# Kernel tuning notes

Measured on AMD Instinct MI355X. Metric: run time of the kernel, lower is better.

The kernel has to match this reference:

```python
import jax, jax.numpy as jnp
import numpy as np

B, T, J, C = 8, 243, 17, 512
H = 8
HD = C // H  # 64
SCALE = HD ** -0.5


def setup_inputs() -> dict:
    key = jax.random.key(0)
    ks = jax.random.split(key, 6)
    x = jax.random.normal(ks[0], (B, T, J, C), dtype=jnp.float32)
    # external attention map, broadcast-compatible with [B,H,J,T,T]; make it row-normalized like a softmax
    am = jax.random.uniform(ks[1], (B, H, J, T, T), dtype=jnp.float32)
    att_map = am / jnp.sum(am, axis=-1, keepdims=True)
    weight = jax.random.uniform(ks[2], (1,), dtype=jnp.float32)
    w_qkv = jax.random.normal(ks[3], (3 * C, C), dtype=jnp.float32) * 0.02
    w_proj = jax.random.normal(ks[4], (C, C), dtype=jnp.float32) * 0.02
    b_proj = jax.random.normal(ks[5], (C,), dtype=jnp.float32) * 0.02
    return {"x": x, "att_map": att_map, "weight": weight,
            "w_qkv": w_qkv, "w_proj": w_proj, "b_proj": b_proj}


def reference(x, att_map, weight, w_qkv, w_proj, b_proj):
    b, t, j, c = x.shape
    h, hd = H, c // H
    # qkv projection (no bias): [B,T,J,3C] -> [3,B,H,T,J,hd]
    qkv = jnp.einsum('btjc,dc->btjd', x, w_qkv).reshape(b, t, j, 3, h, hd)
    qkv = jnp.transpose(qkv, (3, 0, 4, 1, 2, 5))
    q, k, v = qkv[0], qkv[1], qkv[2]
    # transpose T <-> J: attention runs over the temporal axis per joint
    qt = jnp.swapaxes(q, 2, 3)  # [B,H,J,T,hd]
    kt = jnp.swapaxes(k, 2, 3)
    vt = jnp.swapaxes(v, 2, 3)
    attn = jnp.einsum('bhjtc,bhjsc->bhjts', qt, kt) * SCALE  # [B,H,J,T,T]
    attn = jax.nn.softmax(attn, axis=-1)
    # blend with external attention map (dropout p=0.0 -> identity)
    attn = weight * attn + (1.0 - weight) * att_map
    out = jnp.einsum('bhjts,bhjsc->bhjtc', attn, vt)  # [B,H,J,T,hd]
    out = jnp.transpose(out, (0, 3, 2, 1, 4)).reshape(b, t, j, c)  # [B,T,J,C]
    out = out @ w_proj.T + b_proj
    return out
```

## Files before the change

kernel.cpp:

```cpp
#include <hip/hip_runtime.h>
#include <hip/hip_bf16.h>

#define B_ 8
#define T_ 243
#define J_ 17
#define C_ 512
#define H_ 8
#define HD_ 64
#define M_ (B_*T_*J_)
#define SCALE_ 0.125f
#define QKV_ELEMS (B_*H_*J_*T_*HD_)

typedef __attribute__((ext_vector_type(4))) float f32x4;
typedef __attribute__((ext_vector_type(8))) short bf16x8;

__device__ __forceinline__ ushort f2bf(float f) {
  union { float f; unsigned u; } v; v.f = f;
  unsigned r = v.u + 0x7FFFu + ((v.u >> 16) & 1u);
  return (ushort)(r >> 16);
}
__device__ __forceinline__ float bf2f(ushort u) {
  union { unsigned u; float f; } v; v.u = (unsigned)u << 16; return v.f;
}
__device__ __forceinline__ int vchunk(int g, int row) {
  return g ^ (row & 7) ^ ((row >> 3) & 7);
}

__global__ __launch_bounds__(256) void cvt_kernel(const float* __restrict__ in,
                                                  ushort* __restrict__ out, int n8) {
  int i = blockIdx.x * 256 + threadIdx.x;
  if (i >= n8) return;
  const float4* p = (const float4*)in + (size_t)i * 2;
  float4 v0 = p[0], v1 = p[1];
  bf16x8 o;
  o[0] = (short)f2bf(v0.x); o[1] = (short)f2bf(v0.y);
  o[2] = (short)f2bf(v0.z); o[3] = (short)f2bf(v0.w);
  o[4] = (short)f2bf(v1.x); o[5] = (short)f2bf(v1.y);
  o[6] = (short)f2bf(v1.z); o[7] = (short)f2bf(v1.w);
  *(bf16x8*)(out + (size_t)i * 8) = o;
}

template<int EPI>
__global__ __launch_bounds__(256) void gemm_bt(
    const ushort* __restrict__ A, const ushort* __restrict__ Bm,
    ushort* __restrict__ qkvout, float* __restrict__ fout,
    const float* __restrict__ bias)
{
  __shared__ ushort As[128 * 64];
  __shared__ ushort Bs[128 * 64];
  const int tid = threadIdx.x;
  const int lane = tid & 63;
  const int lo = lane & 15, hi = lane >> 4;
  const int wave = tid >> 6;
  const int wr = wave >> 1, wc = wave & 1;
  const int mt = blockIdx.x, nt = blockIdx.y;

  f32x4 acc[4][4] = {};

  for (int ks = 0; ks < 8; ++ks) {
    const int k0 = ks * 64;
    bf16x8 ra[4], rb[4];
    #pragma unroll
    for (int i = 0; i < 4; ++i) {
      int c = tid + i * 256;
      int row = c >> 3, col8 = c & 7;
      int arow = mt * 128 + row; if (arow > M_ - 1) arow = M_ - 1;
      ra[i] = *(const bf16x8*)(A + (size_t)arow * 512 + k0 + col8 * 8);
      int brow = nt * 128 + row;
      rb[i] = *(const bf16x8*)(Bm + (size_t)brow * 512 + k0 + col8 * 8);
    }
    __syncthreads();
    #pragma unroll
    for (int i = 0; i < 4; ++i) {
      int c = tid + i * 256;
      int row = c >> 3, col8 = c & 7;
      int sc = col8 ^ (row & 7);
      *(bf16x8*)(As + row * 64 + sc * 8) = ra[i];
      *(bf16x8*)(Bs + row * 64 + sc * 8) = rb[i];
    }
    __syncthreads();
    #pragma unroll
    for (int kk = 0; kk < 2; ++kk) {
      bf16x8 af[4], bf[4];
      #pragma unroll
      for (int mf = 0; mf < 4; ++mf) {
        int row = wr * 64 + mf * 16 + lo;
        int sc = (kk * 4 + hi) ^ (row & 7);
        af[mf] = *(const bf16x8*)(As + row * 64 + sc * 8);
      }
      #pragma unroll
      for (int nf = 0; nf < 4; ++nf) {
        int row = wc * 64 + nf * 16 + lo;
        int sc = (kk * 4 + hi) ^ (row & 7);
        bf[nf] = *(const bf16x8*)(Bs + row * 64 + sc * 8);
      }
      #pragma unroll
      for (int mf = 0; mf < 4; ++mf)
        #pragma unroll
        for (int nf = 0; nf < 4; ++nf)
          acc[mf][nf] = __builtin_amdgcn_mfma_f32_16x16x32_bf16(af[mf], bf[nf], acc[mf][nf], 0, 0, 0);
    }
  }

  if (EPI == 0) {
    const int which = nt >> 2;
    const int h = (nt * 2 + wc) & 7;
    const float scale = (which == 0) ? SCALE_ : 1.0f;
    ushort* basep = qkvout + (size_t)which * QKV_ELEMS;
    #pragma unroll
    for (int mf = 0; mf < 4; ++mf) {
      #pragma unroll
      for (int i = 0; i < 4; ++i) {
        int r = mt * 128 + wr * 64 + mf * 16 + hi * 4 + i;
        if (r >= M_) continue;
        int b = r / (T_ * J_);
        int rem = r - b * (T_ * J_);
        int t = rem / J_;
        int j = rem - t * J_;
        size_t rowoff = (((size_t)(b * H_ + h) * J_ + j) * T_ + t) * HD_;
        #pragma unroll
        for (int nf = 0; nf < 4; ++nf) {
          int hd = nf * 16 + lo;
          basep[rowoff + hd] = f2bf(acc[mf][nf][i] * scale);
        }
      }
    }
  } else {
    #pragma unroll
    for (int mf = 0; mf < 4; ++mf) {
      #pragma unroll
      for (int i = 0; i < 4; ++i) {
        int r = mt * 128 + wr * 64 + mf * 16 + hi * 4 + i;
        if (r >= M_) continue;
        #pragma unroll
        for (int nf = 0; nf < 4; ++nf) {
          int n = nt * 128 + wc * 64 + nf * 16 + lo;
          fout[(size_t)r * C_ + n] = acc[mf][nf][i] + bias[n];
        }
      }
    }
  }
}

__global__ __launch_bounds__(256, 3) void attn_kernel(
    const ushort* __restrict__ q, const ushort* __restrict__ k,
    const ushort* __restrict__ v, const float* __restrict__ am,
    const float* __restrict__ wptr, ushort* __restrict__ outO)
{
  __shared__ ushort Vt[64 * 256];
  __shared__ ushort Ps[64 * 128];
  __shared__ float red0[2][64];
  __shared__ float red1[2][64];

  const int tid = threadIdx.x;
  const int lane = tid & 63;
  const int lo = lane & 15, hi = lane >> 4;
  const int wave = tid >> 6;
  const int wr = wave >> 1, wc = wave & 1;
  const int bid = blockIdx.x;
  const int workid = (bid & 7) * 544 + (bid >> 3);
  const int bhj = workid >> 2, rt = workid & 3;
  const int bh = bhj / J_, j = bhj - bh * J_;
  const int b = bh >> 3, h = bh & 7;
  const float w = wptr[0];
  const float wb = 1.0f - w;
  const size_t kvbase = (size_t)bhj * (T_ * HD_);
  const int r0 = rt * 64;

  #pragma unroll
  for (int it = 0; it < 8; ++it) {
    int c = tid + it * 256;
    int s = c >> 3, hd0 = (c & 7) * 8;
    bf16x8 val = {};
    if (s < T_) val = *(const bf16x8*)(v + kvbase + (size_t)s * HD_ + hd0);
    #pragma unroll
    for (int e = 0; e < 8; ++e) {
      int row = hd0 + e;
      int chunk = vchunk(s >> 3, row);
      Vt[row * 256 + chunk * 8 + (s & 7)] = (ushort)val[e];
    }
  }
  __syncthreads();

  bf16x8 aq[2][2];
  #pragma unroll
  for (int mf = 0; mf < 2; ++mf) {
    int t = r0 + wr * 32 + mf * 16 + lo; if (t > T_ - 1) t = T_ - 1;
    #pragma unroll
    for (int kk = 0; kk < 2; ++kk)
      aq[mf][kk] = *(const bf16x8*)(q + kvbase + (size_t)t * HD_ + kk * 32 + hi * 8);
  }

  f32x4 acc[2][8] = {};
  #pragma unroll
  for (int nf = 0; nf < 8; ++nf) {
    int s = wc * 128 + nf * 16 + lo; if (s > T_ - 1) s = T_ - 1;
    #pragma unroll
    for (int kk = 0; kk < 2; ++kk) {
      bf16x8 bk = *(const bf16x8*)(k + kvbase + (size_t)s * HD_ + kk * 32 + hi * 8);
      #pragma unroll
      for (int mf = 0; mf < 2; ++mf)
        acc[mf][nf] = __builtin_amdgcn_mfma_f32_16x16x32_bf16(aq[mf][kk], bk, acc[mf][nf], 0, 0, 0);
    }
  }

  float rmax[2][4];
  #pragma unroll
  for (int mf = 0; mf < 2; ++mf)
    #pragma unroll
    for (int i = 0; i < 4; ++i) {
      float m = -1e30f;
      #pragma unroll
      for (int nf = 0; nf < 8; ++nf) {
        int s = wc * 128 + nf * 16 + lo;
        if (s < T_) m = fmaxf(m, acc[mf][nf][i]);
      }
      rmax[mf][i] = m;
    }
  #pragma unroll
  for (int d = 1; d < 16; d <<= 1)
    #pragma unroll
    for (int mf = 0; mf < 2; ++mf)
      #pragma unroll
      for (int i = 0; i < 4; ++i)
        rmax[mf][i] = fmaxf(rmax[mf][i], __shfl_xor(rmax[mf][i], d, 64));
  if (lo == 0) {
    #pragma unroll
    for (int mf = 0; mf < 2; ++mf)
      #pragma unroll
      for (int i = 0; i < 4; ++i)
        red0[wc][wr * 32 + mf * 16 + hi * 4 + i] = rmax[mf][i];
  }
  __syncthreads();

  float rsum[2][4];
  #pragma unroll
  for (int mf = 0; mf < 2; ++mf)
    #pragma unroll
    for (int i = 0; i < 4; ++i) {
      float Mx = fmaxf(rmax[mf][i], red0[wc ^ 1][wr * 32 + mf * 16 + hi * 4 + i]);
      float ssum = 0.f;
      #pragma unroll
      for (int nf = 0; nf < 8; ++nf) {
        int s = wc * 128 + nf * 16 + lo;
        float e = 0.f;
        if (s < T_) e = __expf(acc[mf][nf][i] - Mx);
        acc[mf][nf][i] = e;
        ssum += e;
      }
      rsum[mf][i] = ssum;
    }
  #pragma unroll
  for (int d = 1; d < 16; d <<= 1)
    #pragma unroll
    for (int mf = 0; mf < 2; ++mf)
      #pragma unroll
      for (int i = 0; i < 4; ++i)
        rsum[mf][i] += __shfl_xor(rsum[mf][i], d, 64);
  if (lo == 0) {
    #pragma unroll
    for (int mf = 0; mf < 2; ++mf)
      #pragma unroll
      for (int i = 0; i < 4; ++i)
        red1[wc][wr * 32 + mf * 16 + hi * 4 + i] = rsum[mf][i];
  }
  __syncthreads();

  float pinv[2][4];
  #pragma unroll
  for (int mf = 0; mf < 2; ++mf)
    #pragma unroll
    for (int i = 0; i < 4; ++i) {
      float L = rsum[mf][i] + red1[wc ^ 1][wr * 32 + mf * 16 + hi * 4 + i];
      pinv[mf][i] = w / L;
    }

  f32x4 oacc[2][2] = {};
  #pragma unroll
  for (int h2 = 0; h2 < 2; ++h2) {
    __syncthreads();
    if (wc == h2) {
      #pragma unroll
      for (int mf = 0; mf < 2; ++mf)
        #pragma unroll
        for (int i = 0; i < 4; ++i) {
          int row_local = wr * 32 + mf * 16 + hi * 4 + i;
          float pw = pinv[mf][i];
          #pragma unroll
          for (int nf = 0; nf < 8; ++nf) {
            int s = h2 * 128 + nf * 16 + lo;
            float p = (s < T_) ? acc[mf][nf][i] * pw : 0.f;
            int s_local = nf * 16 + lo;
            int chunk = (s_local >> 3) ^ (row_local & 7);
            Ps[row_local * 128 + chunk * 8 + (s_local & 7)] = f2bf(p);
          }
        }
    }
    __syncthreads();
    #pragma unroll
    for (int kk = 0; kk < 4; ++kk) {
      bf16x8 ap[2], bv[2];
      #pragma unroll
      for (int mf = 0; mf < 2; ++mf) {
        int row = wr * 32 + mf * 16 + lo;
        int chunk = (kk * 4 + hi) ^ (row & 7);
        ap[mf] = *(const bf16x8*)(Ps + row * 128 + chunk * 8);
      }
      #pragma unroll
      for (int nf = 0; nf < 2; ++nf) {
        int row = wc * 32 + nf * 16 + lo;
        int chunk = vchunk((h2 * 4 + kk) * 4 + hi, row);
        bv[nf] = *(const bf16x8*)(Vt + row * 256 + chunk * 8);
      }
      #pragma unroll
      for (int mf = 0; mf < 2; ++mf)
        #pragma unroll
        for (int nf = 0; nf < 2; ++nf)
          oacc[mf][nf] = __builtin_amdgcn_mfma_f32_16x16x32_bf16(ap[mf], bv[nf], oacc[mf][nf], 0, 0, 0);
    }
  }

  const float* amrow[2];
  #pragma unroll
  for (int mf = 0; mf < 2; ++mf) {
    int t = r0 + wr * 32 + mf * 16 + lo; if (t > T_ - 1) t = T_ - 1;
    amrow[mf] = am + (size_t)bhj * (T_ * T_) + (size_t)t * T_;
  }
  f32x4 amacc[2][2] = {};
  #pragma unroll
  for (int kk = 0; kk < 8; ++kk) {
    const int s8 = kk * 32 + hi * 8;
    bf16x8 aa[2];
    #pragma unroll
    for (int mf = 0; mf < 2; ++mf) {
      bf16x8 r;
      if (s8 + 7 <= T_ - 1) {
        #pragma unroll
        for (int e = 0; e < 8; ++e) r[e] = (short)f2bf(amrow[mf][s8 + e]);
      } else {
        #pragma unroll
        for (int e = 0; e < 8; ++e) {
          int s = s8 + e;
          r[e] = (s <= T_ - 1) ? (short)f2bf(amrow[mf][s]) : (short)0;
        }
      }
      aa[mf] = r;
    }
    bf16x8 bv[2];
    #pragma unroll
    for (int nf = 0; nf < 2; ++nf) {
      int row = wc * 32 + nf * 16 + lo;
      int chunk = vchunk(kk * 4 + hi, row);
      bv[nf] = *(const bf16x8*)(Vt + row * 256 + chunk * 8);
    }
    #pragma unroll
    for (int mf = 0; mf < 2; ++mf)
      #pragma unroll
      for (int nf = 0; nf < 2; ++nf)
        amacc[mf][nf] = __builtin_amdgcn_mfma_f32_16x16x32_bf16(aa[mf], bv[nf], amacc[mf][nf], 0, 0, 0);
  }

  #pragma unroll
  for (int mf = 0; mf < 2; ++mf)
    #pragma unroll
    for (int i = 0; i < 4; ++i) {
      int t = r0 + wr * 32 + mf * 16 + hi * 4 + i;
      if (t >= T_) continue;
      size_t orow = ((size_t)(b * T_ + t) * J_ + j) * C_ + h * HD_;
      #pragma unroll
      for (int nf = 0; nf < 2; ++nf) {
        int hd = wc * 32 + nf * 16 + lo;
        outO[orow + hd] = f2bf(oacc[mf][nf][i] + wb * amacc[mf][nf][i]);
      }
    }
}

extern "C" void kernel_launch(void* const* d_in, const int* in_sizes, int n_in,
                              void* d_out, int out_size, void* d_ws, size_t ws_size,
                              hipStream_t stream) {
  const float* x      = (const float*)d_in[0];
  const float* am     = (const float*)d_in[1];
  const float* weight = (const float*)d_in[2];
  const float* w_qkv  = (const float*)d_in[3];
  const float* w_proj = (const float*)d_in[4];
  const float* b_proj = (const float*)d_in[5];
  float* outp = (float*)d_out;

  char* ws = (char*)d_ws;
  ushort* wqkv_bf  = (ushort*)(ws);
  ushort* wproj_bf = (ushort*)(ws + 1572864);
  ushort* xbf      = (ushort*)(ws + 2097152);
  ushort* qws      = (ushort*)(ws + 35938304);
  ushort* kws = qws + QKV_ELEMS;
  ushort* vws = kws + QKV_ELEMS;
  if (ws_size < 137461760ull) return;

  cvt_kernel<<<8262, 256, 0, stream>>>(x, xbf, 2115072);
  cvt_kernel<<<384, 256, 0, stream>>>(w_qkv, wqkv_bf, 98304);
  cvt_kernel<<<128, 256, 0, stream>>>(w_proj, wproj_bf, 32768);

  gemm_bt<0><<<dim3(259, 12), 256, 0, stream>>>(xbf, wqkv_bf, qws, nullptr, nullptr);

  attn_kernel<<<4352, 256, 0, stream>>>(qws, kws, vws, am, weight, xbf);

  gemm_bt<1><<<dim3(259, 4), 256, 0, stream>>>(xbf, wproj_bf, nullptr, outp, b_proj);
}
```

Measured before the change: 336.9 us.

## Process 128 query rows per 512-thread attention block and use packed bf16 convert

The attention kernel now uses 512-thread blocks that each cover 128 query rows instead of 64, so each V tile staged into shared memory is reused by twice as many rows and the grid is halved. The P·V stage is split into four phases with a smaller 128x64 P buffer, which adds more block-wide barriers. The external attention-map conversion now uses the v_cvt_pk_bf16_f32 instruction to pack two floats per instruction instead of manual rounding. Occupancy and register pressure change with the new launch bounds, and the shown parts of the softmax section may need matching updates that are not visible here.

```diff
diff --git a/kernel.cpp b/kernel.cpp
--- a/kernel.cpp
+++ b/kernel.cpp
@@ -18,9 +18,6 @@
   union { float f; unsigned u; } v; v.f = f;
   unsigned r = v.u + 0x7FFFu + ((v.u >> 16) & 1u);
   return (ushort)(r >> 16);
-}
-__device__ __forceinline__ float bf2f(ushort u) {
-  union { unsigned u; float f; } v; v.u = (unsigned)u << 16; return v.f;
 }
 __device__ __forceinline__ int vchunk(int g, int row) {
   return g ^ (row & 7) ^ ((row >> 3) & 7);
@@ -142,34 +139,35 @@
   }
 }
 
-__global__ __launch_bounds__(256, 3) void attn_kernel(
+__global__ __launch_bounds__(512, 6) void attn_kernel(
     const ushort* __restrict__ q, const ushort* __restrict__ k,
     const ushort* __restrict__ v, const float* __restrict__ am,
     const float* __restrict__ wptr, ushort* __restrict__ outO)
 {
   __shared__ ushort Vt[64 * 256];
-  __shared__ ushort Ps[64 * 128];
-  __shared__ float red0[2][64];
-  __shared__ float red1[2][64];
+  __shared__ ushort Ps[128 * 64];
+  __shared__ float red0[2][128];
+  __shared__ float red1[2][128];
 
   const int tid = threadIdx.x;
   const int lane = tid & 63;
   const int lo = lane & 15, hi = lane >> 4;
   const int wave = tid >> 6;
-  const int wr = wave >> 1, wc = wave & 1;
+  const int wr = wave >> 1;
+  const int wc = wave & 1;
   const int bid = blockIdx.x;
-  const int workid = (bid & 7) * 544 + (bid >> 3);
-  const int bhj = workid >> 2, rt = workid & 3;
+  const int workid = (bid & 7) * 272 + (bid >> 3);
+  const int bhj = workid >> 1, rt2 = workid & 1;
   const int bh = bhj / J_, j = bhj - bh * J_;
   const int b = bh >> 3, h = bh & 7;
   const float w = wptr[0];
   const float wb = 1.0f - w;
   const size_t kvbase = (size_t)bhj * (T_ * HD_);
-  const int r0 = rt * 64;
-
-  #pragma unroll
-  for (int it = 0; it < 8; ++it) {
-    int c = tid + it * 256;
+  const int r0 = rt2 * 128;
+
+  #pragma unroll
+  for (int it = 0; it < 4; ++it) {
+    int c = tid + it * 512;
     int s = c >> 3, hd0 = (c & 7) * 8;
     bf16x8 val = {};
     if (s < T_) val = *(const bf16x8*)(v + kvbase + (size_t)s * HD_ + hd0);
@@ -277,9 +275,10 @@
 
   f32x4 oacc[2][2] = {};
   #pragma unroll
-  for (int h2 = 0; h2 < 2; ++h2) {
+  for (int ph = 0; ph < 4; ++ph) {
     __syncthreads();
-    if (wc == h2) {
+    if (wc == (ph >> 1)) {
+      const int nfbase = (ph & 1) * 4;
       #pragma unroll
       for (int mf = 0; mf < 2; ++mf)
         #pragma unroll
@@ -287,30 +286,31 @@
           int row_local = wr * 32 + mf * 16 + hi * 4 + i;
           float pw = pinv[mf][i];
           #pragma unroll
-          for (int nf = 0; nf < 8; ++nf) {
-            int s = h2 * 128 + nf * 16 + lo;
-            float p = (s < T_) ? acc[mf][nf][i] * pw : 0.f;
-            int s_local = nf * 16 + lo;
+          for (int nf = 0; nf < 4; ++nf) {
+            int nfg = nfbase + nf;
+            int s = wc * 128 + nfg * 16 + lo;
+            float p = (s < T_) ? acc[mf][nfg][i] * pw : 0.f;
+            int s_local = (nfg & 3) * 16 + lo;
             int chunk = (s_local >> 3) ^ (row_local & 7);
-            Ps[row_local * 128 + chunk * 8 + (s_local & 7)] = f2bf(p);
+            Ps[row_local * 64 + chunk * 8 + (s_local & 7)] = f2bf(p);
           }
         }
     }
     __syncthreads();
     #pragma unroll
-    for (int kk = 0; kk < 4; ++kk) {
+    for (int kk = 0; kk < 2; ++kk) {
       bf16x8 ap[2], bv[2];
       #pragma unroll
       for (int mf = 0; mf < 2; ++mf) {
         int row = wr * 32 + mf * 16 + lo;
         int chunk = (kk * 4 + hi) ^ (row & 7);
-        ap[mf] = *(const bf16x8*)(Ps + row * 128 + chunk * 8);
+        ap[mf] = *(const bf16x8*)(Ps + row * 64 + chunk * 8);
       }
       #pragma unroll
       for (int nf = 0; nf < 2; ++nf) {
         int row = wc * 32 + nf * 16 + lo;
-        int chunk = vchunk((h2 * 4 + kk) * 4 + hi, row);
-        bv[nf] = *(const bf16x8*)(Vt + row * 256 + chunk * 8);
+        int g = ph * 8 + kk * 4 + hi;
+        bv[nf] = *(const bf16x8*)(Vt + row * 256 + vchunk(g, row) * 8);
       }
       #pragma unroll
       for (int mf = 0; mf < 2; ++mf)
@@ -333,25 +333,29 @@
     bf16x8 aa[2];
     #pragma unroll
     for (int mf = 0; mf < 2; ++mf) {
-      bf16x8 r;
+      float fv[8];
       if (s8 + 7 <= T_ - 1) {
         #pragma unroll
-        for (int e = 0; e < 8; ++e) r[e] = (short)f2bf(amrow[mf][s8 + e]);
+        for (int e = 0; e < 8; ++e) fv[e] = amrow[mf][s8 + e];
       } else {
         #pragma unroll
         for (int e = 0; e < 8; ++e) {
           int s = s8 + e;
-          r[e] = (s <= T_ - 1) ? (short)f2bf(amrow[mf][s]) : (short)0;
+          fv[e] = (s <= T_ - 1) ? amrow[mf][s] : 0.f;
         }
       }
-      aa[mf] = r;
+      union { bf16x8 v; unsigned u[4]; } r;
+      #pragma unroll
+      for (int e2 = 0; e2 < 4; ++e2)
+        asm("v_cvt_pk_bf16_f32 %0, %1, %2" : "=v"(r.u[e2]) : "v"(fv[e2 * 2]), "v"(fv[e2 * 2 + 1]));
+      aa[mf] = r.v;
     }
     bf16x8 bv[2];
     #pragma unroll
     for (int nf = 0; nf < 2; ++nf) {
       int row = wc * 32 + nf * 16 + lo;
-      int chunk = vchunk(kk * 4 + hi, row);
-      bv[nf] = *(const bf16x8*)(Vt + row * 256 + chunk * 8);
+      int g = kk * 4 + hi;
+      bv[nf] = *(const bf16x8*)(Vt + row * 256 + vchunk(g, row) * 8);
     }
     #pragma unroll
     for (int mf = 0; mf < 2; ++mf)
@@ -401,7 +405,7 @@
 
   gemm_bt<0><<<dim3(259, 12), 256, 0, stream>>>(xbf, wqkv_bf, qws, nullptr, nullptr);
 
-  attn_kernel<<<4352, 256, 0, stream>>>(qws, kws, vws, am, weight, xbf);
+  attn_kernel<<<2176, 512, 0, stream>>>(qws, kws, vws, am, weight, xbf);
 
   gemm_bt<1><<<dim3(259, 4), 256, 0, stream>>>(xbf, wproj_bf, nullptr, outp, b_proj);
 }
```

Measured after the change: 589.5 us. 1.75x slower.
